# Kernel optimization log

Hardware: AMD Instinct MI355X
Metric: run time of the kernel (lower is better)

## Reference

```python
import jax, jax.numpy as jnp
import numpy as np

N_NODES = 100000
N_EDGES = 3200000
D_IN = 128
D_HID = 128
N_CLASSES = 40


def setup_inputs() -> dict:
    key = jax.random.key(0)
    ks = jax.random.split(key, 8)
    x = jax.random.normal(ks[0], (N_NODES, D_IN), dtype=jnp.float32)
    edge_index = jax.random.randint(ks[1], (2, N_EDGES), 0, N_NODES, dtype=jnp.int64)
    s1 = 1.0 / np.sqrt(D_IN)
    s2 = 1.0 / np.sqrt(D_HID)
    W1 = jax.random.normal(ks[2], (D_IN, D_HID), dtype=jnp.float32) * s1
    b1 = jnp.zeros((D_HID,), dtype=jnp.float32)
    W2 = jax.random.normal(ks[3], (D_HID, D_HID), dtype=jnp.float32) * s2
    b2 = jnp.zeros((D_HID,), dtype=jnp.float32)
    Wl = jax.random.normal(ks[4], (D_HID, N_CLASSES), dtype=jnp.float32) * s2
    bl = jnp.zeros((N_CLASSES,), dtype=jnp.float32)
    return {"x": x, "edge_index": edge_index, "W1": W1, "b1": b1,
            "W2": W2, "b2": b2, "Wl": Wl, "bl": bl}


def _gcn_conv(x, W, b, src, dst, inv_sqrt_deg, n_nodes):
    # h = X @ W  (linear transform first: cheaper when out_dim <= in_dim)
    h = x @ W  # [N, d_out]
    # symmetric normalization: norm_e = deg(src)^-1/2 * deg(dst)^-1/2
    norm = inv_sqrt_deg[src] * inv_sqrt_deg[dst]  # [E]
    msg = h[src] * norm[:, None]                  # gather + scale  [E, d_out]
    out = jax.ops.segment_sum(msg, dst, num_segments=n_nodes)  # scatter-add
    return out + b


def reference(x, edge_index, W1, b1, W2, b2, Wl, bl):
    n = x.shape[0]
    # GCNConv adds self-loops before normalization (PyG default)
    loops = jnp.arange(n, dtype=edge_index.dtype)
    src = jnp.concatenate([edge_index[0], loops])
    dst = jnp.concatenate([edge_index[1], loops])
    deg = jax.ops.segment_sum(jnp.ones_like(dst, dtype=x.dtype), dst, num_segments=n)
    inv_sqrt_deg = jnp.where(deg > 0, jax.lax.rsqrt(deg), 0.0)

    h = _gcn_conv(x, W1, b1, src, dst, inv_sqrt_deg, n)
    h = jax.nn.relu(h)
    h = _gcn_conv(h, W2, b2, src, dst, inv_sqrt_deg, n)
    h = jax.nn.relu(h)
    return h @ Wl + bl
```

## Files before the change

kernel.cpp:

```cpp
#include <hip/hip_runtime.h>
#include <hip/hip_bf16.h>

typedef _Float16 f16;
typedef _Float16 f16x4 __attribute__((ext_vector_type(4)));
typedef _Float16 f16x8 __attribute__((ext_vector_type(8)));
typedef float f32x4 __attribute__((ext_vector_type(4)));

#define D 128
#define N_CLS 40
#define BN 128
#define NBMAX 1024


__global__ __launch_bounds__(256) void k_hist(const int* __restrict__ dst,
                                              int* __restrict__ bcnt, int e) {
  __shared__ int lh[NBMAX];
  for (int j = threadIdx.x; j < NBMAX; j += 256) lh[j] = 0;
  __syncthreads();
  int stride = gridDim.x * blockDim.x;
  for (int q = blockIdx.x * blockDim.x + threadIdx.x; q < e; q += stride)
    atomicAdd(&lh[dst[q] >> 7], 1);
  __syncthreads();
  for (int j = threadIdx.x; j < NBMAX; j += 256)
    if (lh[j]) atomicAdd(&bcnt[j], lh[j]);
}

__global__ __launch_bounds__(1024) void k_bscan(const int* __restrict__ bcnt,
                                                int* __restrict__ bbase,
                                                int* __restrict__ bcur) {
  __shared__ int sums[NBMAX];
  int t = threadIdx.x;
  int c = bcnt[t];
  sums[t] = c;
  __syncthreads();
  for (int off = 1; off < NBMAX; off <<= 1) {
    int a = (t >= off) ? sums[t - off] : 0;
    __syncthreads();
    sums[t] += a;
    __syncthreads();
  }
  bbase[t] = sums[t] - c;
  bcur[t] = sums[t] - c;
}

__global__ __launch_bounds__(256) void k_place(const int* __restrict__ src,
                                               const int* __restrict__ dst,
                                               int* __restrict__ bcur,
                                               unsigned int* __restrict__ binned,
                                               int e, int nwg) {
  __shared__ int lh[NBMAX];
  __shared__ int lofs[NBMAX];
  __shared__ int lcur[NBMAX];
  int chunk = (e + nwg - 1) / nwg;
  int lo = blockIdx.x * chunk;
  int hi = min(e, lo + chunk);
  int t = threadIdx.x;
  for (int j = t; j < NBMAX; j += 256) { lh[j] = 0; lcur[j] = 0; }
  __syncthreads();
  for (int q = lo + t; q < hi; q += 256) atomicAdd(&lh[dst[q] >> 7], 1);
  __syncthreads();
  for (int j = t; j < NBMAX; j += 256) {
    int c = lh[j];
    lofs[j] = c ? atomicAdd(&bcur[j], c) : 0;
  }
  __syncthreads();
  for (int q = lo + t; q < hi; q += 256) {
    int d = dst[q];
    int b = d >> 7;
    int r = atomicAdd(&lcur[b], 1);
    binned[lofs[b] + r] = ((unsigned int)(d & 127) << 17) | (unsigned int)src[q];
  }
}

__global__ __launch_bounds__(256) void k_csr(const unsigned int* __restrict__ binned,
                                             const int* __restrict__ bbase,
                                             int* __restrict__ csr,
                                             int* __restrict__ deg,
                                             float* __restrict__ isd,
                                             int* __restrict__ row_start, int n) {
  int b = blockIdx.x;
  int lo = bbase[b], hi = bbase[b + 1];
  __shared__ int h[BN];
  __shared__ int sc[BN];
  __shared__ int cur[BN];
  int t = threadIdx.x;
  if (t < BN) h[t] = 0;
  __syncthreads();
  for (int q = lo + t; q < hi; q += 256) atomicAdd(&h[binned[q] >> 17], 1);
  __syncthreads();
  if (t < BN) sc[t] = h[t];
  __syncthreads();
  for (int off = 1; off < BN; off <<= 1) {
    int a = 0;
    if (t < BN && t >= off) a = sc[t - off];
    __syncthreads();
    if (t < BN) sc[t] += a;
    __syncthreads();
  }
  if (t < BN) {
    int excl = sc[t] - h[t];
    cur[t] = lo + excl;
    int i = b * BN + t;
    if (i < n) {
      deg[i] = h[t];
      isd[i] = rsqrtf((float)(h[t] + 1));
      row_start[i] = lo + excl;
    }
  }
  __syncthreads();
  for (int q = lo + t; q < hi; q += 256) {
    unsigned int u = binned[q];
    int p = atomicAdd(&cur[u >> 17], 1);
    csr[p] = (int)(u & 0x1FFFF);
  }
}

__global__ __launch_bounds__(256) void k_wt(const float* __restrict__ W1,
                                            const float* __restrict__ W2,
                                            f16* __restrict__ O1,
                                            f16* __restrict__ O2) {
  const float* W = blockIdx.x ? W2 : W1;
  f16* O = blockIdx.x ? O2 : O1;
  __shared__ f16 lt[D][136];
  int t = threadIdx.x;
  for (int q = t; q < D * D; q += 256) {
    int k = q >> 7, c = q & 127;
    lt[c][k] = (f16)W[q];
  }
  __syncthreads();
  for (int q = t; q < D * 16; q += 256) {
    int row = q >> 4, cb = (q & 15) << 3;
    *(f16x8*)(O + ((size_t)row << 7) + cb) = *(const f16x8*)&lt[row][cb];
  }
}

template <bool HALF_IN>
__global__ __launch_bounds__(256) void k_gemm_m(const void* __restrict__ Xv,
                                                const f16* __restrict__ Wtr,
                                                const float* __restrict__ isd,
                                                f16* __restrict__ HS, int n) {
  __shared__ f16 Wt[D][136];
  __shared__ f16 ot[64][136];
  const size_t ss = (size_t)n * 32;
  int t = threadIdx.x;
  int r0 = blockIdx.x * 64;
  for (int q = t; q < D * 16; q += 256) {
    int row = q >> 4, cb = (q & 15) << 3;
    *(f16x8*)&Wt[row][cb] = *(const f16x8*)(Wtr + ((size_t)row << 7) + cb);
  }
  __syncthreads();

  int wave = t >> 6, lane = t & 63;
  int lw = lane & 15, kg = lane >> 4;
  int arow = r0 + (wave << 4) + lw;
  if (arow >= n) arow = n - 1;
  f32x4 acc[8];
#pragma unroll
  for (int ct = 0; ct < 8; ++ct) acc[ct] = (f32x4)0.f;
#pragma unroll
  for (int ks = 0; ks < 4; ++ks) {
    f16x8 af;
    if (HALF_IN) {
      af = *(const f16x8*)((const f16*)Xv + (size_t)arow * D + ks * 32 + kg * 8);
    } else {
      const float* xp = (const float*)Xv + (size_t)arow * D + ks * 32 + kg * 8;
      float4 x0 = *(const float4*)xp;
      float4 x1 = *(const float4*)(xp + 4);
      af[0] = (f16)x0.x; af[1] = (f16)x0.y; af[2] = (f16)x0.z; af[3] = (f16)x0.w;
      af[4] = (f16)x1.x; af[5] = (f16)x1.y; af[6] = (f16)x1.z; af[7] = (f16)x1.w;
    }
#pragma unroll
    for (int ct = 0; ct < 8; ++ct) {
      f16x8 bf = *(const f16x8*)&Wt[ct * 16 + lw][ks * 32 + kg * 8];
      acc[ct] = __builtin_amdgcn_mfma_f32_16x16x32_f16(af, bf, acc[ct], 0, 0, 0);
    }
  }
  int lrow = (wave << 4) + (kg << 2);
  float sv[4];
#pragma unroll
  for (int rr = 0; rr < 4; ++rr) {
    int node = r0 + lrow + rr;
    sv[rr] = isd[node < n ? node : n - 1];
  }
#pragma unroll
  for (int ct = 0; ct < 8; ++ct)
#pragma unroll
    for (int rr = 0; rr < 4; ++rr)
      ot[lrow + rr][ct * 16 + lw] = (f16)(acc[ct][rr] * sv[rr]);
  __syncthreads();
  {
    int orow = t >> 2, cb = (t & 3) << 3;
    if (r0 + orow < n) {
#pragma unroll
      for (int s = 0; s < 4; ++s)
        *(f16x8*)(HS + (size_t)s * ss + (size_t)(r0 + orow) * 32 + cb) =
            *(const f16x8*)&ot[orow][s * 32 + cb];
    }
  }
}

__device__ inline f16x8 shfl_xor_f16x8(f16x8 v, int m) {
  union { f16x8 h; int i[4]; } u;
  u.h = v;
#pragma unroll
  for (int k = 0; k < 4; ++k) u.i[k] = __shfl_xor(u.i[k], m);
  return u.h;
}

__global__ __launch_bounds__(256) void k_aggs(const f16* __restrict__ HS,
                                              const int* __restrict__ csr,
                                              const int* __restrict__ row_start,
                                              const int* __restrict__ deg,
                                              const float* __restrict__ bias,
                                              f16* __restrict__ G, int n) {
  const size_t ss = (size_t)n * 32;
  int t = threadIdx.x;
  int wave = t >> 6, lane = t & 63;
  int g = lane >> 4, r = lane & 15;
  int s = blockIdx.x & 3;
  int i0 = ((blockIdx.x >> 2) << 4) + (wave << 2) + g;
  bool ok = i0 < n;
  int i = ok ? i0 : n - 1;
  int q = r & 3, er = r >> 2;
  int dg = deg[i];
  const int* cp = csr + row_start[i];
  const char* sbase = (const char*)(HS + (size_t)s * ss);
  unsigned qofs = (unsigned)(q << 4);
  f16x8 a0 = (f16x8)0, a1 = (f16x8)0, a2 = (f16x8)0, a3 = (f16x8)0;
  int iA = cp[er];
  int iB = cp[er + 4];
  int iC = cp[er + 8];
  int iD = cp[er + 12];
  for (int u = 0; u < dg; u += 16) {
    unsigned oA = ((unsigned)iA << 6) + qofs;
    unsigned oB = ((unsigned)iB << 6) + qofs;
    unsigned oC = ((unsigned)iC << 6) + qofs;
    unsigned oD = ((unsigned)iD << 6) + qofs;
    iA = cp[u + 16 + er];
    iB = cp[u + 20 + er];
    iC = cp[u + 24 + er];
    iD = cp[u + 28 + er];
    if (u + er < dg)
      a0 += *(const f16x8*)(sbase + oA);
    if (u + 4 + er < dg)
      a1 += *(const f16x8*)(sbase + oB);
    if (u + 8 + er < dg)
      a2 += *(const f16x8*)(sbase + oC);
    if (u + 12 + er < dg)
      a3 += *(const f16x8*)(sbase + oD);
  }
  f16x8 tv = (a0 + a1) + (a2 + a3);
  tv += shfl_xor_f16x8(tv, 4);
  tv += shfl_xor_f16x8(tv, 8);
  f16x8 svv = *(const f16x8*)(sbase + ((unsigned)i << 6) + qofs);
  float di = rsqrtf((float)(dg + 1));
  const float* bp = bias + s * 32 + (q << 3);
  float4 b0 = *(const float4*)bp;
  float4 b1 = *(const float4*)(bp + 4);
  float bv[8] = {b0.x, b0.y, b0.z, b0.w, b1.x, b1.y, b1.z, b1.w};
  f16x8 ov;
#pragma unroll
  for (int j = 0; j < 8; ++j) {
    float v = di * ((float)tv[j] + (float)svv[j]) + bv[j];
    v = v > 0.f ? v : 0.f;
    ov[j] = (f16)v;
  }
  if (ok && er == 0)
    *(f16x8*)(G + (size_t)i * D + s * 32 + (q << 3)) = ov;
}

__global__ __launch_bounds__(256) void k_cls(const f16* __restrict__ H,
                                             const float* __restrict__ Wl,
                                             const float* __restrict__ bl,
                                             float* __restrict__ out, int n) {
  __shared__ float wt[N_CLS][D];
  int t = threadIdx.x;
  for (int q = t; q < D * N_CLS; q += 256) {
    int k = q / N_CLS, c = q - k * N_CLS;
    wt[c][k] = Wl[q];
  }
  int wv = t >> 6, lane = t & 63, g = lane >> 4, l = lane & 15;
  float bb0 = bl[l];
  float bb1 = bl[16 + l];
  float bb2 = (l < 8) ? bl[32 + l] : 0.f;
  __syncthreads();
  int node0 = (blockIdx.x << 7) + (wv << 2) + g;
  for (int it = 0; it < 8; ++it) {
    int node = node0 + it * 16;
    if (node >= n) break;
    f16x8 h = *(const f16x8*)(H + (size_t)node * D + l * 8);
    float hf[8];
#pragma unroll
    for (int j = 0; j < 8; ++j) hf[j] = (float)h[j];
    float r0 = bb0, r1 = bb1, r2 = bb2;
#pragma unroll 4
    for (int c = 0; c < N_CLS; ++c) {
      const float* wp = &wt[c][l * 8];
      float4 w0 = *(const float4*)wp;
      float4 w1 = *(const float4*)(wp + 4);
      float p = hf[0] * w0.x + hf[1] * w0.y + hf[2] * w0.z + hf[3] * w0.w +
                hf[4] * w1.x + hf[5] * w1.y + hf[6] * w1.z + hf[7] * w1.w;
      p += __shfl_xor(p, 1);
      p += __shfl_xor(p, 2);
      p += __shfl_xor(p, 4);
      p += __shfl_xor(p, 8);
      if ((c & 15) == l) {
        if (c < 16) r0 += p;
        else if (c < 32) r1 += p;
        else r2 += p;
      }
    }
    float* op = out + (size_t)node * N_CLS;
    op[l] = r0;
    op[16 + l] = r1;
    if (l < 8) op[32 + l] = r2;
  }
}

extern "C" void kernel_launch(void* const* d_in, const int* in_sizes, int n_in,
                              void* d_out, int out_size, void* d_ws, size_t ws_size,
                              hipStream_t stream) {
  const float* x  = (const float*)d_in[0];
  const int*   ei = (const int*)d_in[1];
  const float* W1 = (const float*)d_in[2];
  const float* b1 = (const float*)d_in[3];
  const float* W2 = (const float*)d_in[4];
  const float* b2 = (const float*)d_in[5];
  const float* Wl = (const float*)d_in[6];
  const float* bl = (const float*)d_in[7];
  float* out = (float*)d_out;

  const int n = in_sizes[0] / D;
  const int e = in_sizes[1] / 2;
  const int* src = ei;
  const int* dst = ei + e;
  const int nb = (n + BN - 1) / BN;

  char* ws = (char*)d_ws;
  size_t off = 0;
  auto alloc = [&](size_t bytes) -> void* {
    void* p = ws + off;
    off += (bytes + 255) & ~(size_t)255;
    return p;
  };
  int*   bcnt      = (int*)alloc(NBMAX * 4);
  int*   bbase     = (int*)alloc(NBMAX * 4);
  int*   bcur      = (int*)alloc(NBMAX * 4);
  int*   deg       = (int*)alloc((size_t)n * 4);
  int*   row_start = (int*)alloc((size_t)n * 4);
  float* isd       = (float*)alloc((size_t)n * 4);
  int*   csr       = (int*)alloc(((size_t)e + 64) * 4);
  f16*   Wt1       = (f16*)alloc((size_t)D * D * 2);
  f16*   Wt2       = (f16*)alloc((size_t)D * D * 2);
  f16*   hA        = (f16*)alloc((size_t)n * D * 2);
  f16*   hB        = (f16*)alloc((size_t)n * D * 2);
  unsigned int* binned = (unsigned int*)hA;

  hipMemsetAsync(bcnt, 0, NBMAX * 4, stream);
  hipMemsetAsync(csr + e, 0, 64 * 4, stream);

  const int nwg_place = 512;
  k_hist<<<1024, 256, 0, stream>>>(dst, bcnt, e);
  k_bscan<<<1, 1024, 0, stream>>>(bcnt, bbase, bcur);
  k_place<<<nwg_place, 256, 0, stream>>>(src, dst, bcur, binned, e, nwg_place);
  k_csr<<<nb, 256, 0, stream>>>(binned, bbase, csr, deg, isd, row_start, n);
  k_wt<<<2, 256, 0, stream>>>(W1, W2, Wt1, Wt2);

  int gblocks = (n + 63) / 64;
  int ablocks = ((n + 15) / 16) * 4;
  k_gemm_m<false><<<gblocks, 256, 0, stream>>>(x, Wt1, isd, hA, n);
  k_aggs<<<ablocks, 256, 0, stream>>>(hA, csr, row_start, deg, b1, hB, n);
  k_gemm_m<true><<<gblocks, 256, 0, stream>>>(hB, Wt2, isd, hA, n);
  k_aggs<<<ablocks, 256, 0, stream>>>(hA, csr, row_start, deg, b2, hB, n);
  k_cls<<<(n + 127) / 128, 256, 0, stream>>>(hB, Wl, bl, out, n);
}
```

Baseline: 594.7 us.

## Replace atomic bin placement with per-block histogram and column prefix scan

The binning preprocessing now writes a per-workgroup bucket histogram (2048 chunks × 1024 buckets) and computes each block's bucket offsets with a column-wise exclusive scan kernel. The old version used global atomics on bucket cursors and recounted dst inside the place kernel. The place kernel now just reads its precomputed offsets, which removes the second histogram pass over dst and the global atomics. This also makes placement deterministic. In exchange it adds an extra kernel and roughly 8 MB of histogram traffic, stored in the hB buffer.

```diff
diff --git a/kernel.cpp b/kernel.cpp
--- a/kernel.cpp
+++ b/kernel.cpp
@@ -10,24 +10,48 @@
 #define N_CLS 40
 #define BN 128
 #define NBMAX 1024
-
-
-__global__ __launch_bounds__(256) void k_hist(const int* __restrict__ dst,
-                                              int* __restrict__ bcnt, int e) {
+#define G_PRE 2048
+
+
+__global__ __launch_bounds__(256) void k_hist2(const int* __restrict__ dst,
+                                               int* __restrict__ bh, int e) {
   __shared__ int lh[NBMAX];
-  for (int j = threadIdx.x; j < NBMAX; j += 256) lh[j] = 0;
-  __syncthreads();
-  int stride = gridDim.x * blockDim.x;
-  for (int q = blockIdx.x * blockDim.x + threadIdx.x; q < e; q += stride)
-    atomicAdd(&lh[dst[q] >> 7], 1);
-  __syncthreads();
-  for (int j = threadIdx.x; j < NBMAX; j += 256)
-    if (lh[j]) atomicAdd(&bcnt[j], lh[j]);
+  int b = blockIdx.x, t = threadIdx.x;
+  for (int j = t; j < NBMAX; j += 256) lh[j] = 0;
+  __syncthreads();
+  int chunk = (e + G_PRE - 1) / G_PRE;
+  int lo = b * chunk, hi = min(e, lo + chunk);
+  for (int q = lo + t; q < hi; q += 256) atomicAdd(&lh[dst[q] >> 7], 1);
+  __syncthreads();
+  for (int j = t; j < NBMAX; j += 256) bh[(size_t)b * NBMAX + j] = lh[j];
+}
+
+__global__ __launch_bounds__(256) void k_lofs(int* __restrict__ bh,
+                                              int* __restrict__ bcnt) {
+  int j = blockIdx.x, t = threadIdx.x;
+  __shared__ int s[256];
+  int v[8];
+#pragma unroll
+  for (int k = 0; k < 8; ++k) v[k] = bh[(size_t)(t * 8 + k) * NBMAX + j];
+  int tt = 0;
+#pragma unroll
+  for (int k = 0; k < 8; ++k) { int x = v[k]; v[k] = tt; tt += x; }
+  s[t] = tt;
+  __syncthreads();
+  for (int off = 1; off < 256; off <<= 1) {
+    int a = (t >= off) ? s[t - off] : 0;
+    __syncthreads();
+    s[t] += a;
+    __syncthreads();
+  }
+  int ex = s[t] - tt;
+  if (t == 255) bcnt[j] = s[255];
+#pragma unroll
+  for (int k = 0; k < 8; ++k) bh[(size_t)(t * 8 + k) * NBMAX + j] = ex + v[k];
 }
 
 __global__ __launch_bounds__(1024) void k_bscan(const int* __restrict__ bcnt,
-                                                int* __restrict__ bbase,
-                                                int* __restrict__ bcur) {
+                                                int* __restrict__ bbase) {
   __shared__ int sums[NBMAX];
   int t = threadIdx.x;
   int c = bcnt[t];
@@ -40,46 +64,41 @@
     __syncthreads();
   }
   bbase[t] = sums[t] - c;
-  bcur[t] = sums[t] - c;
-}
-
-__global__ __launch_bounds__(256) void k_place(const int* __restrict__ src,
-                                               const int* __restrict__ dst,
-                                               int* __restrict__ bcur,
-                                               unsigned int* __restrict__ binned,
-                                               int e, int nwg) {
-  __shared__ int lh[NBMAX];
+}
+
+__global__ __launch_bounds__(256) void k_place3(const int* __restrict__ src,
+                                                const int* __restrict__ dst,
+                                                const int* __restrict__ bh,
+                                                const int* __restrict__ bbase,
+                                                unsigned int* __restrict__ binned,
+                                                int e) {
   __shared__ int lofs[NBMAX];
   __shared__ int lcur[NBMAX];
-  int chunk = (e + nwg - 1) / nwg;
-  int lo = blockIdx.x * chunk;
-  int hi = min(e, lo + chunk);
-  int t = threadIdx.x;
-  for (int j = t; j < NBMAX; j += 256) { lh[j] = 0; lcur[j] = 0; }
-  __syncthreads();
-  for (int q = lo + t; q < hi; q += 256) atomicAdd(&lh[dst[q] >> 7], 1);
-  __syncthreads();
+  int b = blockIdx.x, t = threadIdx.x;
   for (int j = t; j < NBMAX; j += 256) {
-    int c = lh[j];
-    lofs[j] = c ? atomicAdd(&bcur[j], c) : 0;
-  }
-  __syncthreads();
+    lofs[j] = bh[(size_t)b * NBMAX + j] + bbase[j];
+    lcur[j] = 0;
+  }
+  __syncthreads();
+  int chunk = (e + G_PRE - 1) / G_PRE;
+  int lo = b * chunk, hi = min(e, lo + chunk);
   for (int q = lo + t; q < hi; q += 256) {
     int d = dst[q];
-    int b = d >> 7;
-    int r = atomicAdd(&lcur[b], 1);
-    binned[lofs[b] + r] = ((unsigned int)(d & 127) << 17) | (unsigned int)src[q];
+    int bb = d >> 7;
+    int r = atomicAdd(&lcur[bb], 1);
+    binned[lofs[bb] + r] = ((unsigned int)(d & 127) << 17) | (unsigned int)src[q];
   }
 }
 
 __global__ __launch_bounds__(256) void k_csr(const unsigned int* __restrict__ binned,
                                              const int* __restrict__ bbase,
+                                             const int* __restrict__ bcnt,
                                              int* __restrict__ csr,
                                              int* __restrict__ deg,
                                              float* __restrict__ isd,
                                              int* __restrict__ row_start, int n) {
   int b = blockIdx.x;
-  int lo = bbase[b], hi = bbase[b + 1];
+  int lo = bbase[b], hi = lo + bcnt[b];
   __shared__ int h[BN];
   __shared__ int sc[BN];
   __shared__ int cur[BN];
@@ -345,7 +364,6 @@
   };
   int*   bcnt      = (int*)alloc(NBMAX * 4);
   int*   bbase     = (int*)alloc(NBMAX * 4);
-  int*   bcur      = (int*)alloc(NBMAX * 4);
   int*   deg       = (int*)alloc((size_t)n * 4);
   int*   row_start = (int*)alloc((size_t)n * 4);
   float* isd       = (float*)alloc((size_t)n * 4);
@@ -355,15 +373,15 @@
   f16*   hA        = (f16*)alloc((size_t)n * D * 2);
   f16*   hB        = (f16*)alloc((size_t)n * D * 2);
   unsigned int* binned = (unsigned int*)hA;
-
-  hipMemsetAsync(bcnt, 0, NBMAX * 4, stream);
+  int*   bh        = (int*)hB;
+
   hipMemsetAsync(csr + e, 0, 64 * 4, stream);
 
-  const int nwg_place = 512;
-  k_hist<<<1024, 256, 0, stream>>>(dst, bcnt, e);
-  k_bscan<<<1, 1024, 0, stream>>>(bcnt, bbase, bcur);
-  k_place<<<nwg_place, 256, 0, stream>>>(src, dst, bcur, binned, e, nwg_place);
-  k_csr<<<nb, 256, 0, stream>>>(binned, bbase, csr, deg, isd, row_start, n);
+  k_hist2<<<G_PRE, 256, 0, stream>>>(dst, bh, e);
+  k_lofs<<<NBMAX, 256, 0, stream>>>(bh, bcnt);
+  k_bscan<<<1, 1024, 0, stream>>>(bcnt, bbase);
+  k_place3<<<G_PRE, 256, 0, stream>>>(src, dst, bh, bbase, binned, e);
+  k_csr<<<nb, 256, 0, stream>>>(binned, bbase, bcnt, csr, deg, isd, row_start, n);
   k_wt<<<2, 256, 0, stream>>>(W1, W2, Wt1, Wt2);
 
   int gblocks = (n + 63) / 64;
```

New measurement: 608.9 us. 1.02x slower.
